# Kernel tuning notes

Measured on AMD Instinct MI355X. Metric: run time of the kernel, lower is better.

The kernel has to match this reference:

```python
import jax, jax.numpy as jnp
import numpy as np

B, T, C, H = 8, 2048, 1024, 16
S = C // H
LN_EPS = 1e-5


def setup_inputs() -> dict:
    key = jax.random.key(0)
    ks = jax.random.split(key, 12)
    w = lambda k: jax.random.normal(k, (C, C), dtype=jnp.float32) * 0.02
    return {
        "x": jax.random.normal(ks[0], (B, T, C), dtype=jnp.float32),
        "time_mix_k": jax.random.uniform(ks[1], (1, 1, C), dtype=jnp.float32),
        "time_mix_v": jax.random.uniform(ks[2], (1, 1, C), dtype=jnp.float32),
        "time_mix_r": jax.random.uniform(ks[3], (1, 1, C), dtype=jnp.float32),
        # keep exp(time_decay) < 1 for numerical stability over T=2048 steps
        "time_decay": -jax.random.uniform(ks[4], (H, S), minval=0.1, maxval=5.0, dtype=jnp.float32),
        "time_first": jax.random.uniform(ks[5], (H, S), dtype=jnp.float32),
        "Wk": w(ks[6]), "Wv": w(ks[7]), "Wr": w(ks[8]), "Wo": w(ks[9]),
        "ln_g": jnp.ones((C,), jnp.float32),
        "ln_b": jnp.zeros((C,), jnp.float32),
    }


def reference(x, time_mix_k, time_mix_v, time_mix_r, time_decay, time_first, Wk, Wv, Wr, Wo, ln_g, ln_b):
    Bx, Tx, Cx = x.shape
    # time_shift: xx[t] = x[t-1], xx[0] = 0
    xx = jnp.pad(x, ((0, 0), (1, 0), (0, 0)))[:, :-1]
    xk = x * time_mix_k + xx * (1 - time_mix_k)
    xv = x * time_mix_v + xx * (1 - time_mix_v)
    xr = x * time_mix_r + xx * (1 - time_mix_r)
    proj = lambda z, W: jnp.einsum('btc,dc->btd', z, W).reshape(Bx, Tx, H, S)
    k = proj(xk, Wk)  # [B,T,H,S]
    v = proj(xv, Wv)
    r = proj(xr, Wr)
    kv = k * v  # elementwise per-channel 'at' (diagonal of outer-product state)
    decay = jnp.exp(time_decay)  # [H,S]

    def step(state, inp):
        kv_t, r_t = inp  # [B,H,S] each
        state = kv_t + decay * state
        o = r_t * (time_first * kv_t + state)
        return state, o

    kvT = jnp.swapaxes(kv, 0, 1)  # [T,B,H,S]
    rT = jnp.swapaxes(r, 0, 1)
    _, outT = jax.lax.scan(step, jnp.zeros((Bx, H, S), x.dtype), (kvT, rT))
    out = jnp.swapaxes(outT, 0, 1).reshape(Bx, Tx, Cx)
    mu = out.mean(-1, keepdims=True)
    var = out.var(-1, keepdims=True)
    out = (out - mu) / jnp.sqrt(var + LN_EPS) * ln_g + ln_b
    return jnp.einsum('btc,dc->btd', out, Wo)
```

## Files before the change

kernel.cpp:

```cpp
#include <hip/hip_runtime.h>

#define Bsz 8
#define Tn  2048
#define Cn  1024
#define Hn  16
#define Sn  64
#define Mn  (Bsz * Tn)
#define NC  32
#define LCH (Tn / NC)
#define Kd  1024
#define NKT (Kd / 64)

typedef __attribute__((ext_vector_type(8))) short bf16x8;
typedef __attribute__((ext_vector_type(4))) float f32x4;

__device__ __forceinline__ unsigned short f2bf(float f) {
  union { float f; unsigned int u; } v;
  v.f = f;
  unsigned int r = (v.u + 0x7FFFu + ((v.u >> 16) & 1u)) >> 16;
  return (unsigned short)r;
}
__device__ __forceinline__ float bf2f(unsigned short u) {
  union { unsigned int u; float f; } v;
  v.u = ((unsigned int)u) << 16;
  return v.f;
}

__global__ void wconv_kernel(const float* __restrict__ Wk, const float* __restrict__ Wv,
                             const float* __restrict__ Wr, const float* __restrict__ Wo,
                             unsigned short* __restrict__ out) {
  int i = blockIdx.x * blockDim.x + threadIdx.x;
  int which = i >> 18;
  int off = (i & 0x3FFFF) * 4;
  const float* src = which == 0 ? Wk : which == 1 ? Wv : which == 2 ? Wr : Wo;
  float4 f = *(const float4*)(src + off);
  ushort4 o;
  o.x = f2bf(f.x); o.y = f2bf(f.y); o.z = f2bf(f.z); o.w = f2bf(f.w);
  *(ushort4*)(out + (size_t)which * (Cn * Cn) + off) = o;
}

__global__ void mix3_kernel(const float* __restrict__ x,
                            const float* __restrict__ tmk, const float* __restrict__ tmv,
                            const float* __restrict__ tmr,
                            unsigned short* __restrict__ ok, unsigned short* __restrict__ ov,
                            unsigned short* __restrict__ orr) {
  int idx = blockIdx.x * blockDim.x + threadIdx.x;
  int c4 = idx & (Cn / 4 - 1);
  int bt = idx >> 8;
  int t = bt & (Tn - 1);
  size_t base = (size_t)bt * Cn + c4 * 4;
  float4 xv = *(const float4*)(x + base);
  float4 xxv = {0.f, 0.f, 0.f, 0.f};
  if (t != 0) xxv = *(const float4*)(x + base - Cn);
  float4 dx = {xv.x - xxv.x, xv.y - xxv.y, xv.z - xxv.z, xv.w - xxv.w};
  float4 tk = *(const float4*)(tmk + c4 * 4);
  float4 tv = *(const float4*)(tmv + c4 * 4);
  float4 tr = *(const float4*)(tmr + c4 * 4);
  ushort4 a, b, c;
  a.x = f2bf(xxv.x + tk.x * dx.x); a.y = f2bf(xxv.y + tk.y * dx.y);
  a.z = f2bf(xxv.z + tk.z * dx.z); a.w = f2bf(xxv.w + tk.w * dx.w);
  b.x = f2bf(xxv.x + tv.x * dx.x); b.y = f2bf(xxv.y + tv.y * dx.y);
  b.z = f2bf(xxv.z + tv.z * dx.z); b.w = f2bf(xxv.w + tv.w * dx.w);
  c.x = f2bf(xxv.x + tr.x * dx.x); c.y = f2bf(xxv.y + tr.y * dx.y);
  c.z = f2bf(xxv.z + tr.z * dx.z); c.w = f2bf(xxv.w + tr.w * dx.w);
  *(ushort4*)(ok + base) = a;
  *(ushort4*)(ov + base) = b;
  *(ushort4*)(orr + base) = c;
}

__device__ __forceinline__ void gload_lds16(const void* g, void* l) {
  __builtin_amdgcn_global_load_lds((const __attribute__((address_space(1))) void*)g,
                                   (__attribute__((address_space(3))) void*)l, 16, 0, 0);
}

#define LDA(dst, H, KS)                                                            \
  _Pragma("unroll") for (int mi4 = 0; mi4 < 4; ++mi4) {                            \
    const int row = wm * 128 + (H) * 64 + mi4 * 16 + l15;                          \
    dst[mi4] = *(const bf16x8*)(ldsc + dbase + row * 128 +                         \
                                ((((KS) * 4 + lg) ^ (row & 7)) << 4));             \
  }
#define LDB(dst, KS)                                                               \
  _Pragma("unroll") for (int nj = 0; nj < 4; ++nj) {                               \
    const int row = wn * 64 + nj * 16 + l15;                                       \
    dst[nj] = *(const bf16x8*)(ldsc + dbase + 32768 + row * 128 +                  \
                               ((((KS) * 4 + lg) ^ (row & 7)) << 4));              \
  }
#define MFMA16(H, AV, BV)                                                          \
  _Pragma("unroll") for (int mi4 = 0; mi4 < 4; ++mi4)                              \
    _Pragma("unroll") for (int nj = 0; nj < 4; ++nj)                               \
      acc[(H) * 4 + mi4][nj] = __builtin_amdgcn_mfma_f32_16x16x32_bf16(            \
          AV[mi4], BV[nj], acc[(H) * 4 + mi4][nj], 0, 0, 0);

template <bool OUTBF16>
__global__ __launch_bounds__(512, 2) void gemm1b(const unsigned short* __restrict__ A,
                                                 const unsigned short* __restrict__ Bt,
                                                 void* __restrict__ Cm) {
  __shared__ unsigned short lds[65536];
  char* ldsc = (char*)lds;
  const int tid = threadIdx.x;
  const int wid = tid >> 6, lane = tid & 63;
  const int wm = wid >> 2, wn = wid & 3;
  const int l15 = lane & 15, lg = lane >> 4;
  int bid = ((int)blockIdx.x & 7) * 32 + ((int)blockIdx.x >> 3);
  const int mt = bid >> 2, nt = bid & 3;
  const int m0 = mt * 256, n0 = nt * 256;

  const unsigned short* Ag = A + (size_t)m0 * Kd;
  const unsigned short* Bg = Bt + (size_t)n0 * Kd;

  auto stageSlice = [&](const unsigned short* gbase, int ktt, int band, int Loff) {
    const int r = band * 64 + wid * 8 + (lane >> 3);
    const int c = (lane & 7) ^ (r & 7);
    gload_lds16(gbase + (size_t)r * Kd + ktt * 64 + c * 8,
                ldsc + Loff + (band * 64 + wid * 8) * 128 + lane * 16);
  };
  auto stage8 = [&](int ktt, int base) {
#pragma unroll
    for (int band = 0; band < 4; ++band) stageSlice(Ag, ktt, band, base);
#pragma unroll
    for (int band = 0; band < 4; ++band) stageSlice(Bg, ktt, band, base + 32768);
  };

  f32x4 acc[8][4] = {};

  stage8(0, 0);
  __syncthreads();

#pragma unroll 2
  for (int kt = 0; kt < NKT; ++kt) {
    const int dbase = (kt & 1) << 16;
    const int nd = dbase ^ 65536;
    if (kt + 1 < NKT) stage8(kt + 1, nd);

    bf16x8 a0[4], a1[4], a2[4], a3[4], b0[4], b1[4];
    LDA(a0, 0, 0)
    LDB(b0, 0)
    LDA(a1, 1, 0)
    MFMA16(0, a0, b0)
    LDA(a2, 1, 1)
    LDB(b1, 1)
    MFMA16(1, a1, b0)
    LDA(a3, 0, 1)
    MFMA16(1, a2, b1)
    MFMA16(0, a3, b1)

    __syncthreads();
  }

  if (OUTBF16) {
    char* tb = ldsc + wid * 16384;
#pragma unroll
    for (int mi = 0; mi < 8; ++mi)
#pragma unroll
      for (int nj = 0; nj < 4; ++nj)
#pragma unroll
        for (int rr = 0; rr < 4; ++rr) {
          const int row = mi * 16 + lg * 4 + rr;
          const int col = nj * 16 + l15;
          *(unsigned short*)(tb + row * 128 + ((col * 2) ^ ((row & 7) << 4))) =
              f2bf(acc[mi][nj][rr]);
        }
    asm volatile("s_waitcnt lgkmcnt(0)" ::: "memory");
    __builtin_amdgcn_sched_barrier(0);
    const int orl = lane >> 3, och = lane & 7;
#pragma unroll
    for (int it = 0; it < 16; ++it) {
      const int row = it * 8 + orl;
      uint4 vv = *(const uint4*)(tb + row * 128 + ((och * 16) ^ ((row & 7) << 4)));
      const int gr = m0 + wm * 128 + row;
      const int gc = n0 + wn * 64 + och * 8;
      *(uint4*)((unsigned short*)Cm + (size_t)gr * Cn + gc) = vv;
    }
  } else {
#pragma unroll
    for (int mi = 0; mi < 8; ++mi)
#pragma unroll
      for (int nj = 0; nj < 4; ++nj)
#pragma unroll
        for (int rr = 0; rr < 4; ++rr) {
          const int row = m0 + wm * 128 + mi * 16 + lg * 4 + rr;
          const int col = n0 + wn * 64 + nj * 16 + l15;
          ((float*)Cm)[(size_t)row * Cn + col] = acc[mi][nj][rr];
        }
  }
}

__global__ void scan_phase1(const unsigned short* __restrict__ k,
                            const unsigned short* __restrict__ v,
                            const float* __restrict__ td, float* __restrict__ cs) {
  int blk = blockIdx.x;
  int c = blk & (NC - 1);
  int bh = blk >> 5;
  int b = bh >> 4;
  int h = bh & 15;
  int s = threadIdx.x;
  float decay = expf(td[h * Sn + s]);
  size_t base = ((size_t)(b * Tn + c * LCH)) * Cn + h * Sn + s;
  float st = 0.f;
#pragma unroll 8
  for (int i = 0; i < LCH; ++i) {
    float kv = bf2f(k[base]) * bf2f(v[base]);
    st = kv + decay * st;
    base += Cn;
  }
  cs[(size_t)blk * Sn + s] = st;
}

__global__ void scan_phase2(const float* __restrict__ td, float* __restrict__ cs) {
  int bh = blockIdx.x;
  int h = bh & 15;
  int s = threadIdx.x;
  float dL = expf(td[h * Sn + s] * (float)LCH);
  float carry = 0.f;
  for (int c = 0; c < NC; ++c) {
    size_t idx = ((size_t)bh * NC + c) * Sn + s;
    float sc = cs[idx];
    cs[idx] = carry;
    carry = sc + dL * carry;
  }
}

__global__ void scan_phase3(const unsigned short* __restrict__ k,
                            const unsigned short* __restrict__ v,
                            const unsigned short* __restrict__ r,
                            const float* __restrict__ td, const float* __restrict__ tf,
                            const float* __restrict__ cs,
                            unsigned short* __restrict__ out) {
  int blk = blockIdx.x;
  int c = blk & (NC - 1);
  int bh = blk >> 5;
  int b = bh >> 4;
  int h = bh & 15;
  int s = threadIdx.x;
  float decay = expf(td[h * Sn + s]);
  float first = tf[h * Sn + s];
  float st = cs[(size_t)blk * Sn + s];
  size_t base = ((size_t)(b * Tn + c * LCH)) * Cn + h * Sn + s;
#pragma unroll 8
  for (int i = 0; i < LCH; ++i) {
    float kv = bf2f(k[base]) * bf2f(v[base]);
    st = kv + decay * st;
    out[base] = f2bf(bf2f(r[base]) * (first * kv + st));
    base += Cn;
  }
}

__global__ __launch_bounds__(256) void ln_kernel(const unsigned short* __restrict__ in,
                                                 const float* __restrict__ g,
                                                 const float* __restrict__ bb,
                                                 unsigned short* __restrict__ out) {
  int row = blockIdx.x;
  int tid = threadIdx.x;
  size_t base = (size_t)row * Cn + tid * 4;
  ushort4 uv = *(const ushort4*)(in + base);
  float4 xv = {bf2f(uv.x), bf2f(uv.y), bf2f(uv.z), bf2f(uv.w)};
  float sum = xv.x + xv.y + xv.z + xv.w;
  float ss = xv.x * xv.x + xv.y * xv.y + xv.z * xv.z + xv.w * xv.w;
#pragma unroll
  for (int off = 32; off >= 1; off >>= 1) {
    sum += __shfl_down(sum, off, 64);
    ss += __shfl_down(ss, off, 64);
  }
  __shared__ float s1[4], s2[4];
  if ((tid & 63) == 0) { s1[tid >> 6] = sum; s2[tid >> 6] = ss; }
  __syncthreads();
  sum = s1[0] + s1[1] + s1[2] + s1[3];
  ss = s2[0] + s2[1] + s2[2] + s2[3];
  float mu = sum * (1.f / Cn);
  float var = ss * (1.f / Cn) - mu * mu;
  float rstd = rsqrtf(var + 1e-5f);
  float4 gv = *(const float4*)(g + tid * 4);
  float4 bv = *(const float4*)(bb + tid * 4);
  ushort4 o;
  o.x = f2bf((xv.x - mu) * rstd * gv.x + bv.x);
  o.y = f2bf((xv.y - mu) * rstd * gv.y + bv.y);
  o.z = f2bf((xv.z - mu) * rstd * gv.z + bv.z);
  o.w = f2bf((xv.w - mu) * rstd * gv.w + bv.w);
  *(ushort4*)(out + base) = o;
}

extern "C" void kernel_launch(void* const* d_in, const int* in_sizes, int n_in,
                              void* d_out, int out_size, void* d_ws, size_t ws_size,
                              hipStream_t stream) {
  const float* x   = (const float*)d_in[0];
  const float* tmk = (const float*)d_in[1];
  const float* tmv = (const float*)d_in[2];
  const float* tmr = (const float*)d_in[3];
  const float* td  = (const float*)d_in[4];
  const float* tf  = (const float*)d_in[5];
  const float* Wk  = (const float*)d_in[6];
  const float* Wv  = (const float*)d_in[7];
  const float* Wr  = (const float*)d_in[8];
  const float* Wo  = (const float*)d_in[9];
  const float* lng = (const float*)d_in[10];
  const float* lnb = (const float*)d_in[11];
  float* out = (float*)d_out;

  char* ws = (char*)d_ws;
  const size_t MB = 1024 * 1024;
  unsigned short* wbf  = (unsigned short*)(ws);
  unsigned short* xk   = (unsigned short*)(ws + 8 * MB);
  unsigned short* xv_  = (unsigned short*)(ws + 40 * MB);
  unsigned short* xr   = (unsigned short*)(ws + 72 * MB);
  unsigned short* bufK = (unsigned short*)(ws + 104 * MB);
  unsigned short* bufV = (unsigned short*)(ws + 136 * MB);
  unsigned short* bufR = (unsigned short*)(ws + 168 * MB);
  unsigned short* preLN = xk;
  unsigned short* lnout = xv_;
  float* chunkS = (float*)(ws + 200 * MB);

  const int gemm_grid = (Mn / 256) * (Cn / 256);
  const int mix_grid = Mn * (Cn / 4) / 256;

  wconv_kernel<<<4 * Cn * Cn / 4 / 256, 256, 0, stream>>>(Wk, Wv, Wr, Wo, wbf);
  mix3_kernel<<<mix_grid, 256, 0, stream>>>(x, tmk, tmv, tmr, xk, xv_, xr);

  gemm1b<true><<<gemm_grid, 512, 0, stream>>>(xk,  wbf + 0 * (size_t)Cn * Cn, bufK);
  gemm1b<true><<<gemm_grid, 512, 0, stream>>>(xv_, wbf + 1 * (size_t)Cn * Cn, bufV);
  gemm1b<true><<<gemm_grid, 512, 0, stream>>>(xr,  wbf + 2 * (size_t)Cn * Cn, bufR);

  scan_phase1<<<Bsz * Hn * NC, 64, 0, stream>>>(bufK, bufV, td, chunkS);
  scan_phase2<<<Bsz * Hn, 64, 0, stream>>>(td, chunkS);
  scan_phase3<<<Bsz * Hn * NC, 64, 0, stream>>>(bufK, bufV, bufR, td, tf, chunkS, preLN);

  ln_kernel<<<Mn, 256, 0, stream>>>(preLN, lng, lnb, lnout);

  gemm1b<false><<<gemm_grid, 512, 0, stream>>>(lnout, wbf + 3 * (size_t)Cn * Cn, out);

  (void)in_sizes; (void)n_in; (void)out_size; (void)ws_size;
}
```

Baseline: 252.1 us.

## Merge K/V/R projection GEMMs into one launch and split-stage the K-loop pipeline

The three input projection GEMMs now run as one 768-block launch that picks the projection from the block index. This raises the number of blocks in flight and removes two launch gaps. The GEMM core is reworked so the next K-tile is staged in two halves interleaved with the MFMA phases. It uses explicit vmcnt waits plus a raw s_barrier instead of a full __syncthreads, and raises wave priority around the MFMA blocks. The aim is better overlap of global-to-LDS loads with compute. The price is more delicate hand-rolled synchronisation on the double buffer.

```diff
diff --git a/kernel.cpp b/kernel.cpp
--- a/kernel.cpp
+++ b/kernel.cpp
@@ -92,62 +92,77 @@
           AV[mi4], BV[nj], acc[(H) * 4 + mi4][nj], 0, 0, 0);
 
 template <bool OUTBF16>
-__global__ __launch_bounds__(512, 2) void gemm1b(const unsigned short* __restrict__ A,
-                                                 const unsigned short* __restrict__ Bt,
-                                                 void* __restrict__ Cm) {
-  __shared__ unsigned short lds[65536];
-  char* ldsc = (char*)lds;
+__device__ __forceinline__ void gemm_core(const unsigned short* __restrict__ Ag,
+                                          const unsigned short* __restrict__ Bg,
+                                          void* __restrict__ Cm,
+                                          char* ldsc) {
   const int tid = threadIdx.x;
   const int wid = tid >> 6, lane = tid & 63;
   const int wm = wid >> 2, wn = wid & 3;
   const int l15 = lane & 15, lg = lane >> 4;
-  int bid = ((int)blockIdx.x & 7) * 32 + ((int)blockIdx.x >> 3);
-  const int mt = bid >> 2, nt = bid & 3;
-  const int m0 = mt * 256, n0 = nt * 256;
-
-  const unsigned short* Ag = A + (size_t)m0 * Kd;
-  const unsigned short* Bg = Bt + (size_t)n0 * Kd;
-
-  auto stageSlice = [&](const unsigned short* gbase, int ktt, int band, int Loff) {
+
+  auto stageS = [&](const unsigned short* gbase, int ktt, int band, int Loff) {
     const int r = band * 64 + wid * 8 + (lane >> 3);
     const int c = (lane & 7) ^ (r & 7);
     gload_lds16(gbase + (size_t)r * Kd + ktt * 64 + c * 8,
                 ldsc + Loff + (band * 64 + wid * 8) * 128 + lane * 16);
   };
-  auto stage8 = [&](int ktt, int base) {
-#pragma unroll
-    for (int band = 0; band < 4; ++band) stageSlice(Ag, ktt, band, base);
-#pragma unroll
-    for (int band = 0; band < 4; ++band) stageSlice(Bg, ktt, band, base + 32768);
-  };
 
   f32x4 acc[8][4] = {};
 
-  stage8(0, 0);
-  __syncthreads();
+#pragma unroll
+  for (int band = 0; band < 4; ++band) stageS(Ag, 0, band, 0);
+#pragma unroll
+  for (int band = 0; band < 4; ++band) stageS(Bg, 0, band, 32768);
 
 #pragma unroll 2
   for (int kt = 0; kt < NKT; ++kt) {
     const int dbase = (kt & 1) << 16;
     const int nd = dbase ^ 65536;
-    if (kt + 1 < NKT) stage8(kt + 1, nd);
-
-    bf16x8 a0[4], a1[4], a2[4], a3[4], b0[4], b1[4];
-    LDA(a0, 0, 0)
-    LDB(b0, 0)
-    LDA(a1, 1, 0)
-    MFMA16(0, a0, b0)
-    LDA(a2, 1, 1)
-    LDB(b1, 1)
-    MFMA16(1, a1, b0)
-    LDA(a3, 0, 1)
-    MFMA16(1, a2, b1)
-    MFMA16(0, a3, b1)
-
+    const bool st = (kt + 1 < NKT);
+
+    if (st) {
+      stageS(Ag, kt + 1, 0, nd);
+      stageS(Ag, kt + 1, 1, nd);
+      stageS(Bg, kt + 1, 0, nd + 32768);
+      stageS(Bg, kt + 1, 1, nd + 32768);
+      asm volatile("s_waitcnt vmcnt(4)" ::: "memory");
+    } else {
+      asm volatile("s_waitcnt vmcnt(0)" ::: "memory");
+    }
+    __builtin_amdgcn_s_barrier();
+    __builtin_amdgcn_sched_barrier(0);
+
+    {
+      bf16x8 a0[4], a1[4], b0[4];
+      LDA(a0, 0, 0)
+      LDA(a1, 1, 0)
+      LDB(b0, 0)
+      __builtin_amdgcn_s_setprio(1);
+      MFMA16(0, a0, b0)
+      MFMA16(1, a1, b0)
+      __builtin_amdgcn_s_setprio(0);
+    }
+    if (st) {
+      stageS(Ag, kt + 1, 2, nd);
+      stageS(Ag, kt + 1, 3, nd);
+      stageS(Bg, kt + 1, 2, nd + 32768);
+      stageS(Bg, kt + 1, 3, nd + 32768);
+    }
+    {
+      bf16x8 a2[4], a3[4], b1[4];
+      LDA(a2, 0, 1)
+      LDA(a3, 1, 1)
+      LDB(b1, 1)
+      __builtin_amdgcn_s_setprio(1);
+      MFMA16(0, a2, b1)
+      MFMA16(1, a3, b1)
+      __builtin_amdgcn_s_setprio(0);
+    }
+  }
+
+  if (OUTBF16) {
     __syncthreads();
-  }
-
-  if (OUTBF16) {
     char* tb = ldsc + wid * 16384;
 #pragma unroll
     for (int mi = 0; mi < 8; ++mi)
@@ -167,8 +182,8 @@
     for (int it = 0; it < 16; ++it) {
       const int row = it * 8 + orl;
       uint4 vv = *(const uint4*)(tb + row * 128 + ((och * 16) ^ ((row & 7) << 4)));
-      const int gr = m0 + wm * 128 + row;
-      const int gc = n0 + wn * 64 + och * 8;
+      const int gr = wm * 128 + row;
+      const int gc = wn * 64 + och * 8;
       *(uint4*)((unsigned short*)Cm + (size_t)gr * Cn + gc) = vv;
     }
   } else {
@@ -178,11 +193,42 @@
       for (int nj = 0; nj < 4; ++nj)
 #pragma unroll
         for (int rr = 0; rr < 4; ++rr) {
-          const int row = m0 + wm * 128 + mi * 16 + lg * 4 + rr;
-          const int col = n0 + wn * 64 + nj * 16 + l15;
+          const int row = wm * 128 + mi * 16 + lg * 4 + rr;
+          const int col = wn * 64 + nj * 16 + l15;
           ((float*)Cm)[(size_t)row * Cn + col] = acc[mi][nj][rr];
         }
   }
+}
+
+__global__ __launch_bounds__(512, 2) void gemmF(const unsigned short* __restrict__ xk,
+                                                const unsigned short* __restrict__ xv,
+                                                const unsigned short* __restrict__ xr,
+                                                const unsigned short* __restrict__ wbf,
+                                                unsigned short* __restrict__ ck,
+                                                unsigned short* __restrict__ cv,
+                                                unsigned short* __restrict__ cr) {
+  __shared__ unsigned short lds[65536];
+  int bid = ((int)blockIdx.x & 7) * 96 + ((int)blockIdx.x >> 3);
+  const int nt = bid & 3;
+  const int g = bid >> 2;
+  const int proj = g >> 6;
+  const int mt = g & 63;
+  const unsigned short* A = proj == 0 ? xk : proj == 1 ? xv : xr;
+  unsigned short* C = proj == 0 ? ck : proj == 1 ? cv : cr;
+  const unsigned short* W = wbf + (size_t)proj * Cn * Cn;
+  gemm_core<true>(A + (size_t)mt * 256 * Kd, W + (size_t)nt * 256 * Kd,
+                  C + (size_t)mt * 256 * Cn + nt * 256, (char*)lds);
+}
+
+__global__ __launch_bounds__(512, 2) void gemmO(const unsigned short* __restrict__ A,
+                                                const unsigned short* __restrict__ W,
+                                                float* __restrict__ C) {
+  __shared__ unsigned short lds[65536];
+  int bid = ((int)blockIdx.x & 7) * 32 + ((int)blockIdx.x >> 3);
+  const int nt = bid & 3;
+  const int mt = bid >> 2;
+  gemm_core<false>(A + (size_t)mt * 256 * Kd, W + (size_t)nt * 256 * Kd,
+                   C + (size_t)mt * 256 * Cn + nt * 256, (char*)lds);
 }
 
 __global__ void scan_phase1(const unsigned short* __restrict__ k,
@@ -309,15 +355,12 @@
   unsigned short* lnout = xv_;
   float* chunkS = (float*)(ws + 200 * MB);
 
-  const int gemm_grid = (Mn / 256) * (Cn / 256);
   const int mix_grid = Mn * (Cn / 4) / 256;
 
   wconv_kernel<<<4 * Cn * Cn / 4 / 256, 256, 0, stream>>>(Wk, Wv, Wr, Wo, wbf);
   mix3_kernel<<<mix_grid, 256, 0, stream>>>(x, tmk, tmv, tmr, xk, xv_, xr);
 
-  gemm1b<true><<<gemm_grid, 512, 0, stream>>>(xk,  wbf + 0 * (size_t)Cn * Cn, bufK);
-  gemm1b<true><<<gemm_grid, 512, 0, stream>>>(xv_, wbf + 1 * (size_t)Cn * Cn, bufV);
-  gemm1b<true><<<gemm_grid, 512, 0, stream>>>(xr,  wbf + 2 * (size_t)Cn * Cn, bufR);
+  gemmF<<<768, 512, 0, stream>>>(xk, xv_, xr, wbf, bufK, bufV, bufR);
 
   scan_phase1<<<Bsz * Hn * NC, 64, 0, stream>>>(bufK, bufV, td, chunkS);
   scan_phase2<<<Bsz * Hn, 64, 0, stream>>>(td, chunkS);
@@ -325,7 +368,7 @@
 
   ln_kernel<<<Mn, 256, 0, stream>>>(preLN, lng, lnb, lnout);
 
-  gemm1b<false><<<gemm_grid, 512, 0, stream>>>(lnout, wbf + 3 * (size_t)Cn * Cn, out);
+  gemmO<<<256, 512, 0, stream>>>(lnout, wbf + 3 * (size_t)Cn * Cn, out);
 
   (void)in_sizes; (void)n_in; (void)out_size; (void)ws_size;
 }
```

Measured after the change: 341.9 us. 35.6% more time.
